# Optimization experiments

Measured on AMD Instinct MI355X. Metric: run time of the kernel, lower is better.

## Reference

```python
import jax, jax.numpy as jnp
import numpy as np

EPS = 1e-5

def _conv3x3(x, w, b):
    # x: [B,C,H,W], w: [O,I,3,3], b: [O]; padding=1 preserves HxW
    y = jax.lax.conv_general_dilated(
        x, w, window_strides=(1, 1), padding=((1, 1), (1, 1)),
        dimension_numbers=('NCHW', 'OIHW', 'NCHW'))
    return y + b[None, :, None, None]

def _instance_norm(x):
    # InstanceNorm2d(affine=False): normalize over spatial dims per (sample, channel)
    mu = jnp.mean(x, axis=(2, 3), keepdims=True)
    var = jnp.var(x, axis=(2, 3), keepdims=True)
    return (x - mu) * jax.lax.rsqrt(var + EPS)

def setup_inputs() -> dict:
    key = jax.random.key(0)
    k1, k2, k3 = jax.random.split(key, 3)
    B, Cin, Cout, H, W = 8, 32, 64, 320, 320
    x = jax.random.normal(k1, (B, Cin, H, W), dtype=jnp.float32)
    w1 = jax.random.normal(k2, (Cout, Cin, 3, 3), dtype=jnp.float32) * (1.0 / np.sqrt(Cin * 9))
    b1 = jnp.zeros((Cout,), dtype=jnp.float32)
    w2 = jax.random.normal(k3, (Cout, Cout, 3, 3), dtype=jnp.float32) * (1.0 / np.sqrt(Cout * 9))
    b2 = jnp.zeros((Cout,), dtype=jnp.float32)
    return {"x": x, "w1": w1, "b1": b1, "w2": w2, "b2": b2}

def reference(x, w1, b1, w2, b2):
    # conv1 -> InstanceNorm -> ReLU -> (Dropout p=0 identity)
    h = jax.nn.relu(_instance_norm(_conv3x3(x, w1, b1)))
    # conv2 -> InstanceNorm -> ReLU -> (Dropout p=0 identity)
    out = jax.nn.relu(_instance_norm(_conv3x3(h, w2, b2)))
    return out
```

## Files before the change

### kernel.cpp

```cpp
#include <hip/hip_runtime.h>

#define HH 320
#define WW 320
#define BB 8
static constexpr float EPS = 1e-5f;

typedef __attribute__((ext_vector_type(8))) short bf16x8;
typedef __attribute__((ext_vector_type(4))) float f32x4;

__device__ inline float bf2f(unsigned short u) {
    union { unsigned int i; float f; } v; v.i = ((unsigned int)u) << 16; return v.f;
}
__device__ inline unsigned short f2bf(float f) {
    union { float f; unsigned int i; } v; v.f = f;
    unsigned int r = v.i + 0x7fffu + ((v.i >> 16) & 1u);
    return (unsigned short)(r >> 16);
}
__device__ inline unsigned int cvtpk(float a, float b) {
    unsigned int r;
    asm volatile("v_cvt_pk_bf16_f32 %0, %1, %2" : "=v"(r) : "v"(a), "v"(b));
    return r;
}
__device__ inline void glds16(const void* g, void* l) {
    __builtin_amdgcn_global_load_lds(
        (const __attribute__((address_space(1))) unsigned int*)g,
        (__attribute__((address_space(3))) unsigned int*)l, 16, 0, 0);
}

__global__ __launch_bounds__(256) void prep_hwc(const float* __restrict__ in,
                                                unsigned short* __restrict__ out)
{
    __shared__ float sT[32][65];
    const int tid = threadIdx.x;
    const int x0  = blockIdx.x * 64;
    const int y   = blockIdx.y;
    const int b   = blockIdx.z;
    for (int e = tid; e < 32 * 64; e += 256) {
        int c = e >> 6, x = e & 63;
        sT[c][x] = in[(((size_t)(b * 32 + c) * HH) + y) * WW + x0 + x];
    }
    __syncthreads();
    for (int e = tid; e < 64 * 32; e += 256) {
        int x = e >> 5, c = e & 31;
        out[((((size_t)b * HH + y) * WW) + x0 + x) * 32 + c] = f2bf(sT[c][x]);
    }
}

__global__ __launch_bounds__(256) void wprep_swz(const float* __restrict__ w1,
                                                 const float* __restrict__ w2,
                                                 unsigned short* __restrict__ wt1,
                                                 unsigned short* __restrict__ wt2)
{
    int i = blockIdx.x * 256 + threadIdx.x;
    if (i < 2304) {
        int s = i & 3, oc = (i >> 2) & 63, kk = i >> 8;
        int icq = s ^ ((oc >> 1) & 3);
        const float* src = w1 + ((size_t)oc * 32 + icq * 8) * 9 + kk;
        unsigned short pk[8];
#pragma unroll
        for (int j = 0; j < 8; ++j) pk[j] = f2bf(src[j * 9]);
        *(bf16x8*)&wt1[(size_t)i * 8] = *(bf16x8*)pk;
    }
    if (i < 4608) {
        int icc = i / 2304, u = i - icc * 2304;
        int s = u & 3, oc = (u >> 2) & 63, kk = u >> 8;
        int icq = s ^ ((oc >> 1) & 3);
        const float* src = w2 + ((size_t)oc * 64 + icc * 32 + icq * 8) * 9 + kk;
        unsigned short pk[8];
#pragma unroll
        for (int j = 0; j < 8; ++j) pk[j] = f2bf(src[j * 9]);
        *(bf16x8*)&wt2[(size_t)i * 8] = *(bf16x8*)pk;
    }
}

__global__ __launch_bounds__(256) void wfold(const unsigned short* __restrict__ wt2,
                                             const float* __restrict__ b2,
                                             const float2* __restrict__ stats1,
                                             unsigned short* __restrict__ wt2b,
                                             float* __restrict__ bias2b)
{
    __shared__ float sMu[64], sR[64];
    __shared__ float sBias[256];
    const int b = blockIdx.x, tid = threadIdx.x;
    if (tid < 64) {
        float2 ms = stats1[b * 64 + tid];
        sMu[tid] = bf2f(f2bf(ms.x));
        sR[tid]  = ms.y;
    }
    __syncthreads();
    const int oc = tid & 63, rep = tid >> 6;
    float bsum = 0.f;
    for (int cs = rep * 2; cs < rep * 2 + 2; ++cs) {
        int icc = cs >> 2, s = cs & 3;
        int icq = s ^ ((oc >> 1) & 3);
        for (int kk = 0; kk < 9; ++kk) {
            size_t u = (size_t)icc * 2304 + kk * 256 + oc * 4 + s;
            bf16x8 v = *(const bf16x8*)&wt2[u * 8];
            unsigned short o8[8];
#pragma unroll
            for (int j = 0; j < 8; ++j) {
                int ic = icc * 32 + icq * 8 + j;
                unsigned short wb = f2bf(bf2f(((unsigned short*)&v)[j]) * sR[ic]);
                o8[j] = wb;
                bsum += bf2f(wb) * sMu[ic];
            }
            *(bf16x8*)&wt2b[((size_t)b * 4608 + u) * 8] = *(bf16x8*)o8;
        }
    }
    sBias[tid] = bsum;
    __syncthreads();
    if (tid < 64) {
        float t = sBias[tid] + sBias[tid + 64] + sBias[tid + 128] + sBias[tid + 192];
        bias2b[b * 64 + tid] = b2[tid] - t;
    }
}

template<int CIN, int NORM>
__global__ __launch_bounds__(256, 3) void conv_mfma(
    const unsigned short* __restrict__ in_hwc,
    const float2* __restrict__ stats_in,
    const unsigned short* __restrict__ wt,
    const float* __restrict__ bias,
    unsigned short* __restrict__ out_hwc,
    float2* __restrict__ partials)
{
    constexpr int ICC = CIN / 32;

    __shared__ __align__(16) char smem[38912];
    unsigned short* sA    = (unsigned short*)smem;
    unsigned short* sW    = (unsigned short*)(smem + 25344);
    float*          sMaxMu= (float*)(smem + 37632);
    unsigned short* sMuBf = (unsigned short*)(smem + 37888);
    float* sRedS  = (float*)smem;
    float* sRedSS = (float*)(smem + 1024);

    const int tid = threadIdx.x;
    const int x0  = blockIdx.x * 64;
    const int y0  = blockIdx.y * 4;
    const int b   = blockIdx.z;
    const int w   = tid >> 6;
    const int l   = tid & 63;
    const int lm  = l & 15;
    const int g   = l >> 4;

    const unsigned short* wtb = NORM ? wt + (size_t)b * 4608 * 8 : wt;
    const float* biasb        = NORM ? bias + b * 64 : bias;

    if (NORM) {
        if (tid < 64) {
            float2 ms = stats_in[b * 64 + tid];
            unsigned short mb = f2bf(ms.x);
            sMuBf[tid]  = mb;
            sMaxMu[tid] = bf2f(mb);
        }
    }

    f32x4 acc[4][4];
#pragma unroll
    for (int fp = 0; fp < 4; ++fp)
#pragma unroll
        for (int fo = 0; fo < 4; ++fo)
            acc[fp][fo] = (f32x4){0.f, 0.f, 0.f, 0.f};

    for (int icc = 0; icc < ICC; ++icc) {
        __syncthreads();

        if (NORM == 0) {
            for (int r = w; r < 6; r += 4) {
                int gy = y0 + r - 1;
                unsigned short* ldsrow = sA + r * 2112;
                if ((unsigned)gy < HH) {
                    const unsigned short* rowbase =
                        in_hwc + ((size_t)(b * HH + gy) * WW) * CIN + icc * 32;
#pragma unroll
                    for (int i = 0; i < 4; ++i) {
                        int u  = 4 + i * 64 + l;
                        int x  = u >> 2;
                        int cs = (u & 3) ^ ((x >> 1) & 3);
                        glds16(rowbase + (size_t)(x0 + x - 1) * CIN + cs * 8,
                               ldsrow + (size_t)(4 + i * 64) * 8);
                    }
                } else {
                    for (int u2 = l; u2 < 264; u2 += 64)
                        *(bf16x8*)(ldsrow + u2 * 8) = (bf16x8){0,0,0,0,0,0,0,0};
                }
            }
            if (tid < 48) {
                int icq = tid & 3, side = (tid >> 2) & 1, r = tid >> 3;
                int xs = side ? 65 : 0;
                int gy = y0 + r - 1, gx = x0 + xs - 1;
                bf16x8 v = (bf16x8){0,0,0,0,0,0,0,0};
                if ((unsigned)gy < HH && (unsigned)gx < WW)
                    v = *(const bf16x8*)&in_hwc[(((size_t)(b * HH + gy) * WW) + gx) * CIN + icc * 32 + icq * 8];
                *(bf16x8*)&sA[(r * 264 + xs * 4 + icq) * 8] = v;
            }
        } else {
#pragma unroll
            for (int k = 0; k < 7; ++k) {
                int e = tid + k * 256;
                if (e < 1584) {
                    int r = e / 264, rem = e - r * 264;
                    int x = rem >> 2, icq = rem & 3;
                    int gy = y0 + r - 1, gx = x0 + x - 1;
                    int c0 = icc * 32 + icq * 8;
                    unsigned int w4[4];
                    if ((unsigned)gy < HH && (unsigned)gx < WW) {
                        bf16x8 v = *(const bf16x8*)&in_hwc[(((size_t)(b * HH + gy) * WW) + gx) * CIN + c0];
#pragma unroll
                        for (int jp = 0; jp < 4; ++jp) {
                            float f0 = fmaxf(bf2f(((unsigned short*)&v)[2 * jp]),     sMaxMu[c0 + 2 * jp]);
                            float f1 = fmaxf(bf2f(((unsigned short*)&v)[2 * jp + 1]), sMaxMu[c0 + 2 * jp + 1]);
                            w4[jp] = cvtpk(f0, f1);
                        }
                    } else {
#pragma unroll
                        for (int jp = 0; jp < 4; ++jp)
                            w4[jp] = (unsigned int)sMuBf[c0 + 2 * jp] |
                                     ((unsigned int)sMuBf[c0 + 2 * jp + 1] << 16);
                    }
                    *(uint4*)&sA[(r * 264 + x * 4 + (icq ^ ((x >> 1) & 3))) * 8] =
                        make_uint4(w4[0], w4[1], w4[2], w4[3]);
                }
            }
        }

#pragma unroll
        for (int kt = 0; kt < 3; ++kt) {
            if (kt > 0) __syncthreads();
            {
                const unsigned short* wsrc = wtb + ((size_t)icc * 2304 + kt * 768) * 8;
#pragma unroll
                for (int k = 0; k < 3; ++k)
                    glds16(wsrc + (size_t)(k * 256 + w * 64 + l) * 8,
                           sW + (size_t)(k * 256 + w * 64) * 8);
            }
            __syncthreads();

            __builtin_amdgcn_s_setprio(1);
#pragma unroll
            for (int kx = 0; kx < 3; ++kx) {
                bf16x8 af[4], bfr[4];
#pragma unroll
                for (int fp = 0; fp < 4; ++fp) {
                    int xl = fp * 16 + lm + kx;
                    int u  = (xl * 4 + g) ^ ((xl >> 1) & 3);
                    af[fp] = *(const bf16x8*)&sA[((w + kt) * 264 + u) * 8];
                }
#pragma unroll
                for (int fo = 0; fo < 4; ++fo) {
                    int ocr = fo * 16 + lm;
                    int p   = (kx * 64 + ocr) * 4 + (g ^ ((ocr >> 1) & 3));
                    bfr[fo] = *(const bf16x8*)&sW[p * 8];
                }
#pragma unroll
                for (int fo = 0; fo < 4; ++fo)
#pragma unroll
                    for (int fp = 0; fp < 4; ++fp)
                        acc[fp][fo] = __builtin_amdgcn_mfma_f32_16x16x32_bf16(
                            bfr[fo], af[fp], acc[fp][fo], 0, 0, 0);
            }
            __builtin_amdgcn_s_setprio(0);
        }
    }

    __syncthreads();

    const int row = y0 + w;
#pragma unroll
    for (int fo = 0; fo < 4; ++fo) {
        float4 b4 = *(const float4*)&biasb[fo * 16 + g * 4];
        float bb[4] = {b4.x, b4.y, b4.z, b4.w};
        float sj[4] = {0,0,0,0}, qj[4] = {0,0,0,0};
#pragma unroll
        for (int fp = 0; fp < 4; ++fp) {
            float v0 = acc[fp][fo][0] + bb[0], v1 = acc[fp][fo][1] + bb[1];
            float v2 = acc[fp][fo][2] + bb[2], v3 = acc[fp][fo][3] + bb[3];
            sj[0] += v0; qj[0] += v0 * v0;  sj[1] += v1; qj[1] += v1 * v1;
            sj[2] += v2; qj[2] += v2 * v2;  sj[3] += v3; qj[3] += v3 * v3;
            uint2 st = make_uint2(cvtpk(v0, v1), cvtpk(v2, v3));
            *(uint2*)&out_hwc[(((size_t)b * HH + row) * WW + x0 + fp * 16 + lm) * 64 + fo * 16 + g * 4] = st;
        }
#pragma unroll
        for (int m = 1; m <= 8; m <<= 1)
#pragma unroll
            for (int j = 0; j < 4; ++j) {
                sj[j] += __shfl_xor(sj[j], m);
                qj[j] += __shfl_xor(qj[j], m);
            }
        if (lm == 0) {
#pragma unroll
            for (int j = 0; j < 4; ++j) {
                sRedS [w * 64 + fo * 16 + g * 4 + j] = sj[j];
                sRedSS[w * 64 + fo * 16 + g * 4 + j] = qj[j];
            }
        }
    }
    __syncthreads();
    if (tid < 64) {
        float S = 0.f, SS = 0.f;
#pragma unroll
        for (int q = 0; q < 4; ++q) { S += sRedS[q * 64 + tid]; SS += sRedSS[q * 64 + tid]; }
        partials[((size_t)b * 400 + blockIdx.y * 5 + blockIdx.x) * 64 + tid] = make_float2(S, SS);
    }
}

__global__ __launch_bounds__(256) void reduce_stats(const float2* __restrict__ partials,
                                                    float2* __restrict__ stats, int count)
{
    const int b  = blockIdx.x;
    const int oc = threadIdx.x & 63;
    const int q  = threadIdx.x >> 6;
    float s = 0.f, ss = 0.f;
    for (int i = q; i < count; i += 4) {
        float2 p = partials[((size_t)b * count + i) * 64 + oc];
        s += p.x; ss += p.y;
    }
    __shared__ float2 red[4][64];
    red[q][oc] = make_float2(s, ss);
    __syncthreads();
    if (threadIdx.x < 64) {
        float S = 0.f, SS = 0.f;
#pragma unroll
        for (int k = 0; k < 4; ++k) { S += red[k][threadIdx.x].x; SS += red[k][threadIdx.x].y; }
        const float n = (float)(HH * WW);
        float mean = S / n;
        float var  = fmaxf(SS / n - mean * mean, 0.f);
        stats[b * 64 + threadIdx.x] = make_float2(mean, rsqrtf(var + EPS));
    }
}

__global__ __launch_bounds__(256) void finalize_t(const unsigned short* __restrict__ h2,
                                                  const float2* __restrict__ stats,
                                                  float* __restrict__ out)
{
    __shared__ float2 sSt[64];
    const int tid = threadIdx.x;
    const int b   = blockIdx.z;
    if (tid < 64) sSt[tid] = stats[b * 64 + tid];
    __syncthreads();
    const int r   = tid >> 6;
    const int px  = tid & 63;
    const int row = blockIdx.y * 4 + r;
    const int x   = blockIdx.x * 64 + px;
    const unsigned short* src = h2 + ((size_t)(b * HH + row) * WW + x) * 64;
    bf16x8 v[8];
#pragma unroll
    for (int cq = 0; cq < 8; ++cq) v[cq] = *(const bf16x8*)(src + cq * 8);
#pragma unroll
    for (int cq = 0; cq < 8; ++cq)
#pragma unroll
        for (int j = 0; j < 8; ++j) {
            int c = cq * 8 + j;
            float2 ms = sSt[c];
            float f = fmaxf((bf2f(((unsigned short*)&v[cq])[j]) - ms.x) * ms.y, 0.f);
            out[((size_t)(b * 64 + c) * HH + row) * WW + x] = f;
        }
}

extern "C" void kernel_launch(void* const* d_in, const int* in_sizes, int n_in,
                              void* d_out, int out_size, void* d_ws, size_t ws_size,
                              hipStream_t stream)
{
    const float* x  = (const float*)d_in[0];
    const float* w1 = (const float*)d_in[1];
    const float* b1 = (const float*)d_in[2];
    const float* w2 = (const float*)d_in[3];
    const float* b2 = (const float*)d_in[4];
    float* out = (float*)d_out;

    char* ws = (char*)d_ws;
    unsigned short* h    = (unsigned short*)ws;
    float2* partials     = (float2*)(ws + 104857600);
    float2* stats1       = (float2*)(ws + 104857600 + 1638400);
    float2* stats2       = (float2*)(ws + 104857600 + 1638400 + 4096);
    unsigned short* reg2 = (unsigned short*)(ws + 104857600 + 1638400 + 8192);
    unsigned short* x_hwc = reg2;
    unsigned short* h2    = reg2;

    char* ob = (char*)d_out + 209715200;
    float*          bias2b = (float*)(ob - 2048);
    unsigned short* wt2b   = (unsigned short*)(ob - 2048 - 589824);
    unsigned short* wt2    = (unsigned short*)(ob - 2048 - 589824 - 73728);
    unsigned short* wt1    = (unsigned short*)(ob - 2048 - 589824 - 73728 - 36864);

    dim3 cgrid(5, 80, BB);

    wprep_swz<<<18, 256, 0, stream>>>(w1, w2, wt1, wt2);
    prep_hwc<<<dim3(5, HH, BB), 256, 0, stream>>>(x, x_hwc);

    conv_mfma<32, 0><<<cgrid, 256, 0, stream>>>(x_hwc, nullptr, wt1, b1, h, partials);
    reduce_stats<<<BB, 256, 0, stream>>>(partials, stats1, 400);
    wfold<<<BB, 256, 0, stream>>>(wt2, b2, stats1, wt2b, bias2b);
    conv_mfma<64, 1><<<cgrid, 256, 0, stream>>>(h, stats1, wt2b, bias2b, h2, partials);
    reduce_stats<<<BB, 256, 0, stream>>>(partials, stats2, 400);
    finalize_t<<<dim3(5, 80, BB), 256, 0, stream>>>(h2, stats2, out);
}
```

Before: 365.5 us.

## Double-buffer conv input and weight slabs and process four row tiles per block

The conv kernel now loops over four 4-row tiles per block (grid y shrinks from 80 to 20) and double-buffers both the activation tile and the weight slab in LDS. The next slab and the next input group are prefetched while MFMAs run on the current one, and for the normalized conv the global loads are held in registers and written to LDS after compute. Per-block statistics are accumulated across tiles, so the partials count drops to 100 per sample. The aim is to hide global load latency and cut the number of barriers per MFMA. The cost is higher LDS use, a lower occupancy hint (2 blocks instead of 3) and fewer blocks in the grid.

```diff
diff --git a/kernel.cpp b/kernel.cpp
--- a/kernel.cpp
+++ b/kernel.cpp
@@ -116,7 +116,7 @@
 }
 
 template<int CIN, int NORM>
-__global__ __launch_bounds__(256, 3) void conv_mfma(
+__global__ __launch_bounds__(256, 2) void conv_mfma(
     const unsigned short* __restrict__ in_hwc,
     const float2* __restrict__ stats_in,
     const unsigned short* __restrict__ wt,
@@ -125,18 +125,19 @@
     float2* __restrict__ partials)
 {
     constexpr int ICC = CIN / 32;
-
-    __shared__ __align__(16) char smem[38912];
-    unsigned short* sA    = (unsigned short*)smem;
-    unsigned short* sW    = (unsigned short*)(smem + 25344);
-    float*          sMaxMu= (float*)(smem + 37632);
-    unsigned short* sMuBf = (unsigned short*)(smem + 37888);
-    float* sRedS  = (float*)smem;
-    float* sRedSS = (float*)(smem + 1024);
+    constexpr int NG  = 4 * ICC;
+    constexpr int NS  = NG * 3;
+
+    __shared__ __align__(16) unsigned short sA[2][6 * 264 * 8];
+    __shared__ __align__(16) unsigned short sWb[2][768 * 8];
+    __shared__ float sRedS[256];
+    __shared__ float sRedSS[256];
+    __shared__ float sMaxMu[64];
+    __shared__ unsigned short sMuBf[64];
 
     const int tid = threadIdx.x;
     const int x0  = blockIdx.x * 64;
-    const int y0  = blockIdx.y * 4;
+    const int yb  = blockIdx.y * 16;
     const int b   = blockIdx.z;
     const int w   = tid >> 6;
     const int l   = tid & 63;
@@ -153,7 +154,101 @@
             sMuBf[tid]  = mb;
             sMaxMu[tid] = bf2f(mb);
         }
-    }
+        __syncthreads();
+    }
+
+    auto stage_slab = [&](int s2, int buf) {
+        int kt2  = s2 % 3;
+        int icc2 = (s2 / 3) % ICC;
+        const unsigned short* wsrc = wtb + ((size_t)icc2 * 2304 + kt2 * 768) * 8;
+        unsigned short* dst = &sWb[buf][0];
+#pragma unroll
+        for (int k = 0; k < 3; ++k)
+            glds16(wsrc + (size_t)(k * 256 + w * 64 + l) * 8,
+                   dst + (size_t)(k * 256 + w * 64) * 8);
+    };
+
+    auto issueA_glds = [&](int gi2) {
+        int t2 = gi2 / ICC, icc2 = gi2 % ICC;
+        int y02 = yb + t2 * 4;
+        unsigned short* buf = &sA[gi2 & 1][0];
+        for (int r = w; r < 6; r += 4) {
+            int gy = y02 + r - 1;
+            unsigned short* ldsrow = buf + r * 2112;
+            if ((unsigned)gy < HH) {
+                const unsigned short* rowbase =
+                    in_hwc + ((size_t)(b * HH + gy) * WW) * CIN + icc2 * 32;
+#pragma unroll
+                for (int i = 0; i < 4; ++i) {
+                    int u  = 4 + i * 64 + l;
+                    int x  = u >> 2;
+                    int cs = (u & 3) ^ ((x >> 1) & 3);
+                    glds16(rowbase + (size_t)(x0 + x - 1) * CIN + cs * 8,
+                           ldsrow + (size_t)(4 + i * 64) * 8);
+                }
+            } else {
+                for (int u2 = l; u2 < 264; u2 += 64)
+                    *(bf16x8*)(ldsrow + u2 * 8) = (bf16x8){0,0,0,0,0,0,0,0};
+            }
+        }
+        if (tid < 48) {
+            int icq = tid & 3, side = (tid >> 2) & 1, r = tid >> 3;
+            int xs = side ? 65 : 0;
+            int gy = y02 + r - 1, gx = x0 + xs - 1;
+            bf16x8 v = (bf16x8){0,0,0,0,0,0,0,0};
+            if ((unsigned)gy < HH && (unsigned)gx < WW)
+                v = *(const bf16x8*)&in_hwc[(((size_t)(b * HH + gy) * WW) + gx) * CIN + icc2 * 32 + icq * 8];
+            *(bf16x8*)&buf[(r * 264 + xs * 4 + icq) * 8] = v;
+        }
+    };
+
+    bf16x8 ld[7];
+    auto issueA_reg = [&](int gi2) {
+        int t2 = gi2 / ICC, icc2 = gi2 % ICC;
+        int y02 = yb + t2 * 4;
+#pragma unroll
+        for (int k = 0; k < 7; ++k) {
+            int e = tid + k * 256;
+            if (e < 1584) {
+                int r = e / 264, rem = e - r * 264;
+                int x = rem >> 2, icq = rem & 3;
+                int gy = y02 + r - 1, gx = x0 + x - 1;
+                if ((unsigned)gy < HH && (unsigned)gx < WW)
+                    ld[k] = *(const bf16x8*)&in_hwc[(((size_t)(b * HH + gy) * WW) + gx) * CIN + icc2 * 32 + icq * 8];
+            }
+        }
+    };
+    auto writeA_reg = [&](int gi2) {
+        int t2 = gi2 / ICC, icc2 = gi2 % ICC;
+        int y02 = yb + t2 * 4;
+        unsigned short* buf = &sA[gi2 & 1][0];
+#pragma unroll
+        for (int k = 0; k < 7; ++k) {
+            int e = tid + k * 256;
+            if (e < 1584) {
+                int r = e / 264, rem = e - r * 264;
+                int x = rem >> 2, icq = rem & 3;
+                int gy = y02 + r - 1, gx = x0 + x - 1;
+                int c0 = icc2 * 32 + icq * 8;
+                unsigned int w4[4];
+                if ((unsigned)gy < HH && (unsigned)gx < WW) {
+#pragma unroll
+                    for (int jp = 0; jp < 4; ++jp) {
+                        float f0 = fmaxf(bf2f(((unsigned short*)&ld[k])[2 * jp]),     sMaxMu[c0 + 2 * jp]);
+                        float f1 = fmaxf(bf2f(((unsigned short*)&ld[k])[2 * jp + 1]), sMaxMu[c0 + 2 * jp + 1]);
+                        w4[jp] = cvtpk(f0, f1);
+                    }
+                } else {
+#pragma unroll
+                    for (int jp = 0; jp < 4; ++jp)
+                        w4[jp] = (unsigned int)sMuBf[c0 + 2 * jp] |
+                                 ((unsigned int)sMuBf[c0 + 2 * jp + 1] << 16);
+                }
+                *(uint4*)&buf[(r * 264 + x * 4 + (icq ^ ((x >> 1) & 3))) * 8] =
+                    make_uint4(w4[0], w4[1], w4[2], w4[3]);
+            }
+        }
+    };
 
     f32x4 acc[4][4];
 #pragma unroll
@@ -162,80 +257,38 @@
         for (int fo = 0; fo < 4; ++fo)
             acc[fp][fo] = (f32x4){0.f, 0.f, 0.f, 0.f};
 
-    for (int icc = 0; icc < ICC; ++icc) {
-        __syncthreads();
-
-        if (NORM == 0) {
-            for (int r = w; r < 6; r += 4) {
-                int gy = y0 + r - 1;
-                unsigned short* ldsrow = sA + r * 2112;
-                if ((unsigned)gy < HH) {
-                    const unsigned short* rowbase =
-                        in_hwc + ((size_t)(b * HH + gy) * WW) * CIN + icc * 32;
-#pragma unroll
-                    for (int i = 0; i < 4; ++i) {
-                        int u  = 4 + i * 64 + l;
-                        int x  = u >> 2;
-                        int cs = (u & 3) ^ ((x >> 1) & 3);
-                        glds16(rowbase + (size_t)(x0 + x - 1) * CIN + cs * 8,
-                               ldsrow + (size_t)(4 + i * 64) * 8);
-                    }
-                } else {
-                    for (int u2 = l; u2 < 264; u2 += 64)
-                        *(bf16x8*)(ldsrow + u2 * 8) = (bf16x8){0,0,0,0,0,0,0,0};
-                }
-            }
-            if (tid < 48) {
-                int icq = tid & 3, side = (tid >> 2) & 1, r = tid >> 3;
-                int xs = side ? 65 : 0;
-                int gy = y0 + r - 1, gx = x0 + xs - 1;
-                bf16x8 v = (bf16x8){0,0,0,0,0,0,0,0};
-                if ((unsigned)gy < HH && (unsigned)gx < WW)
-                    v = *(const bf16x8*)&in_hwc[(((size_t)(b * HH + gy) * WW) + gx) * CIN + icc * 32 + icq * 8];
-                *(bf16x8*)&sA[(r * 264 + xs * 4 + icq) * 8] = v;
-            }
-        } else {
-#pragma unroll
-            for (int k = 0; k < 7; ++k) {
-                int e = tid + k * 256;
-                if (e < 1584) {
-                    int r = e / 264, rem = e - r * 264;
-                    int x = rem >> 2, icq = rem & 3;
-                    int gy = y0 + r - 1, gx = x0 + x - 1;
-                    int c0 = icc * 32 + icq * 8;
-                    unsigned int w4[4];
-                    if ((unsigned)gy < HH && (unsigned)gx < WW) {
-                        bf16x8 v = *(const bf16x8*)&in_hwc[(((size_t)(b * HH + gy) * WW) + gx) * CIN + c0];
-#pragma unroll
-                        for (int jp = 0; jp < 4; ++jp) {
-                            float f0 = fmaxf(bf2f(((unsigned short*)&v)[2 * jp]),     sMaxMu[c0 + 2 * jp]);
-                            float f1 = fmaxf(bf2f(((unsigned short*)&v)[2 * jp + 1]), sMaxMu[c0 + 2 * jp + 1]);
-                            w4[jp] = cvtpk(f0, f1);
-                        }
-                    } else {
-#pragma unroll
-                        for (int jp = 0; jp < 4; ++jp)
-                            w4[jp] = (unsigned int)sMuBf[c0 + 2 * jp] |
-                                     ((unsigned int)sMuBf[c0 + 2 * jp + 1] << 16);
-                    }
-                    *(uint4*)&sA[(r * 264 + x * 4 + (icq ^ ((x >> 1) & 3))) * 8] =
-                        make_uint4(w4[0], w4[1], w4[2], w4[3]);
-                }
-            }
-        }
-
-#pragma unroll
-        for (int kt = 0; kt < 3; ++kt) {
-            if (kt > 0) __syncthreads();
-            {
-                const unsigned short* wsrc = wtb + ((size_t)icc * 2304 + kt * 768) * 8;
-#pragma unroll
-                for (int k = 0; k < 3; ++k)
-                    glds16(wsrc + (size_t)(k * 256 + w * 64 + l) * 8,
-                           sW + (size_t)(k * 256 + w * 64) * 8);
-            }
-            __syncthreads();
-
+    float bb[4][4];
+#pragma unroll
+    for (int fo = 0; fo < 4; ++fo) {
+        float4 b4 = *(const float4*)&biasb[fo * 16 + g * 4];
+        bb[fo][0] = b4.x; bb[fo][1] = b4.y; bb[fo][2] = b4.z; bb[fo][3] = b4.w;
+    }
+    float sjA[4][4] = {}, qjA[4][4] = {};
+
+    stage_slab(0, 0);
+    if (NORM == 0) {
+        issueA_glds(0);
+    } else {
+        issueA_reg(0);
+        writeA_reg(0);
+    }
+    __syncthreads();
+
+    for (int s = 0; s < NS; ++s) {
+        const int kt = s % 3;
+        const int gi = s / 3;
+        const int icc = gi % ICC;
+        const int t  = gi / ICC;
+
+        if (s + 1 < NS) stage_slab(s + 1, (s + 1) & 1);
+        if (kt == 0 && gi + 1 < NG) {
+            if (NORM == 0) issueA_glds(gi + 1);
+            else           issueA_reg(gi + 1);
+        }
+
+        {
+            const unsigned short* bufA = &sA[gi & 1][0];
+            const unsigned short* bufW = &sWb[s & 1][0];
             __builtin_amdgcn_s_setprio(1);
 #pragma unroll
             for (int kx = 0; kx < 3; ++kx) {
@@ -244,13 +297,13 @@
                 for (int fp = 0; fp < 4; ++fp) {
                     int xl = fp * 16 + lm + kx;
                     int u  = (xl * 4 + g) ^ ((xl >> 1) & 3);
-                    af[fp] = *(const bf16x8*)&sA[((w + kt) * 264 + u) * 8];
+                    af[fp] = *(const bf16x8*)(bufA + ((w + kt) * 264 + u) * 8);
                 }
 #pragma unroll
                 for (int fo = 0; fo < 4; ++fo) {
                     int ocr = fo * 16 + lm;
                     int p   = (kx * 64 + ocr) * 4 + (g ^ ((ocr >> 1) & 3));
-                    bfr[fo] = *(const bf16x8*)&sW[p * 8];
+                    bfr[fo] = *(const bf16x8*)(bufW + p * 8);
                 }
 #pragma unroll
                 for (int fo = 0; fo < 4; ++fo)
@@ -261,37 +314,45 @@
             }
             __builtin_amdgcn_s_setprio(0);
         }
-    }
-
-    __syncthreads();
-
-    const int row = y0 + w;
+
+        if (kt == 2 && icc == ICC - 1) {
+            const int row = yb + 4 * t + w;
+#pragma unroll
+            for (int fo = 0; fo < 4; ++fo) {
+#pragma unroll
+                for (int fp = 0; fp < 4; ++fp) {
+                    float v0 = acc[fp][fo][0] + bb[fo][0], v1 = acc[fp][fo][1] + bb[fo][1];
+                    float v2 = acc[fp][fo][2] + bb[fo][2], v3 = acc[fp][fo][3] + bb[fo][3];
+                    sjA[fo][0] += v0; qjA[fo][0] += v0 * v0;
+                    sjA[fo][1] += v1; qjA[fo][1] += v1 * v1;
+                    sjA[fo][2] += v2; qjA[fo][2] += v2 * v2;
+                    sjA[fo][3] += v3; qjA[fo][3] += v3 * v3;
+                    uint2 st = make_uint2(cvtpk(v0, v1), cvtpk(v2, v3));
+                    *(uint2*)&out_hwc[(((size_t)b * HH + row) * WW + x0 + fp * 16 + lm) * 64 + fo * 16 + g * 4] = st;
+                    acc[fp][fo] = (f32x4){0.f, 0.f, 0.f, 0.f};
+                }
+            }
+        }
+
+        if (NORM == 1 && kt == 2 && gi + 1 < NG) writeA_reg(gi + 1);
+
+        __syncthreads();
+    }
+
 #pragma unroll
     for (int fo = 0; fo < 4; ++fo) {
-        float4 b4 = *(const float4*)&biasb[fo * 16 + g * 4];
-        float bb[4] = {b4.x, b4.y, b4.z, b4.w};
-        float sj[4] = {0,0,0,0}, qj[4] = {0,0,0,0};
-#pragma unroll
-        for (int fp = 0; fp < 4; ++fp) {
-            float v0 = acc[fp][fo][0] + bb[0], v1 = acc[fp][fo][1] + bb[1];
-            float v2 = acc[fp][fo][2] + bb[2], v3 = acc[fp][fo][3] + bb[3];
-            sj[0] += v0; qj[0] += v0 * v0;  sj[1] += v1; qj[1] += v1 * v1;
-            sj[2] += v2; qj[2] += v2 * v2;  sj[3] += v3; qj[3] += v3 * v3;
-            uint2 st = make_uint2(cvtpk(v0, v1), cvtpk(v2, v3));
-            *(uint2*)&out_hwc[(((size_t)b * HH + row) * WW + x0 + fp * 16 + lm) * 64 + fo * 16 + g * 4] = st;
-        }
 #pragma unroll
         for (int m = 1; m <= 8; m <<= 1)
 #pragma unroll
             for (int j = 0; j < 4; ++j) {
-                sj[j] += __shfl_xor(sj[j], m);
-                qj[j] += __shfl_xor(qj[j], m);
+                sjA[fo][j] += __shfl_xor(sjA[fo][j], m);
+                qjA[fo][j] += __shfl_xor(qjA[fo][j], m);
             }
         if (lm == 0) {
 #pragma unroll
             for (int j = 0; j < 4; ++j) {
-                sRedS [w * 64 + fo * 16 + g * 4 + j] = sj[j];
-                sRedSS[w * 64 + fo * 16 + g * 4 + j] = qj[j];
+                sRedS [w * 64 + fo * 16 + g * 4 + j] = sjA[fo][j];
+                sRedSS[w * 64 + fo * 16 + g * 4 + j] = qjA[fo][j];
             }
         }
     }
@@ -300,7 +361,7 @@
         float S = 0.f, SS = 0.f;
 #pragma unroll
         for (int q = 0; q < 4; ++q) { S += sRedS[q * 64 + tid]; SS += sRedSS[q * 64 + tid]; }
-        partials[((size_t)b * 400 + blockIdx.y * 5 + blockIdx.x) * 64 + tid] = make_float2(S, SS);
+        partials[((size_t)b * 100 + blockIdx.y * 5 + blockIdx.x) * 64 + tid] = make_float2(S, SS);
     }
 }
 
@@ -383,15 +444,15 @@
     unsigned short* wt2    = (unsigned short*)(ob - 2048 - 589824 - 73728);
     unsigned short* wt1    = (unsigned short*)(ob - 2048 - 589824 - 73728 - 36864);
 
-    dim3 cgrid(5, 80, BB);
+    dim3 cgrid(5, 20, BB);
 
     wprep_swz<<<18, 256, 0, stream>>>(w1, w2, wt1, wt2);
     prep_hwc<<<dim3(5, HH, BB), 256, 0, stream>>>(x, x_hwc);
 
     conv_mfma<32, 0><<<cgrid, 256, 0, stream>>>(x_hwc, nullptr, wt1, b1, h, partials);
-    reduce_stats<<<BB, 256, 0, stream>>>(partials, stats1, 400);
+    reduce_stats<<<BB, 256, 0, stream>>>(partials, stats1, 100);
     wfold<<<BB, 256, 0, stream>>>(wt2, b2, stats1, wt2b, bias2b);
     conv_mfma<64, 1><<<cgrid, 256, 0, stream>>>(h, stats1, wt2b, bias2b, h2, partials);
-    reduce_stats<<<BB, 256, 0, stream>>>(partials, stats2, 400);
+    reduce_stats<<<BB, 256, 0, stream>>>(partials, stats2, 100);
     finalize_t<<<dim3(5, 80, BB), 256, 0, stream>>>(h2, stats2, out);
 }
```

Result: faster. 323.2 us, median of 2 (-11.6%).

## Double-buffer conv1 over 16-row supertiles and fuse stats reduction into weight fold

Applied to the files above, without the earlier changes.

Conv1 now runs as a persistent-style block covering 16 output rows (four 4-row groups). Its input tiles and weight slabs are double-buffered in LDS so the loads for the next step overlap the MFMA work of the current one, and per-block stats partials drop from 400 to 100 per sample. The separate reduce_stats launch for conv1 is merged into the weight-fold kernel, which saves one launch. The cost is that conv1 grid parallelism falls to 800 blocks with higher LDS use (2 waves per SIMD occupancy bound), which may leave CUs underfilled.

```diff
diff --git a/kernel.cpp b/kernel.cpp
--- a/kernel.cpp
+++ b/kernel.cpp
@@ -73,28 +73,46 @@
     }
 }
 
-__global__ __launch_bounds__(256) void wfold(const unsigned short* __restrict__ wt2,
-                                             const float* __restrict__ b2,
-                                             const float2* __restrict__ stats1,
-                                             unsigned short* __restrict__ wt2b,
-                                             float* __restrict__ bias2b)
-{
+__global__ __launch_bounds__(256) void fold_stats(const float2* __restrict__ partials,
+                                                  const float* __restrict__ b2,
+                                                  const unsigned short* __restrict__ wt2,
+                                                  float2* __restrict__ stats1,
+                                                  unsigned short* __restrict__ wt2b,
+                                                  float* __restrict__ bias2b)
+{
+    __shared__ float2 red[4][64];
     __shared__ float sMu[64], sR[64];
     __shared__ float sBias[256];
     const int b = blockIdx.x, tid = threadIdx.x;
+    const int oc = tid & 63, q = tid >> 6;
+
+    float s = 0.f, ss = 0.f;
+    for (int i = q; i < 100; i += 4) {
+        float2 p = partials[((size_t)b * 100 + i) * 64 + oc];
+        s += p.x; ss += p.y;
+    }
+    red[q][oc] = make_float2(s, ss);
+    __syncthreads();
     if (tid < 64) {
-        float2 ms = stats1[b * 64 + tid];
-        sMu[tid] = bf2f(f2bf(ms.x));
-        sR[tid]  = ms.y;
-    }
-    __syncthreads();
-    const int oc = tid & 63, rep = tid >> 6;
+        float S = 0.f, SS = 0.f;
+#pragma unroll
+        for (int k = 0; k < 4; ++k) { S += red[k][tid].x; SS += red[k][tid].y; }
+        const float n = (float)(HH * WW);
+        float mean = S / n;
+        float var  = fmaxf(SS / n - mean * mean, 0.f);
+        float rstd = rsqrtf(var + EPS);
+        stats1[b * 64 + tid] = make_float2(mean, rstd);
+        sMu[tid] = bf2f(f2bf(mean));
+        sR[tid]  = rstd;
+    }
+    __syncthreads();
+
     float bsum = 0.f;
-    for (int cs = rep * 2; cs < rep * 2 + 2; ++cs) {
-        int icc = cs >> 2, s = cs & 3;
-        int icq = s ^ ((oc >> 1) & 3);
+    for (int cs = q * 2; cs < q * 2 + 2; ++cs) {
+        int icc = cs >> 2, sdx = cs & 3;
+        int icq = sdx ^ ((oc >> 1) & 3);
         for (int kk = 0; kk < 9; ++kk) {
-            size_t u = (size_t)icc * 2304 + kk * 256 + oc * 4 + s;
+            size_t u = (size_t)icc * 2304 + kk * 256 + oc * 4 + sdx;
             bf16x8 v = *(const bf16x8*)&wt2[u * 8];
             unsigned short o8[8];
 #pragma unroll
@@ -115,8 +133,176 @@
     }
 }
 
-template<int CIN, int NORM>
-__global__ __launch_bounds__(256, 3) void conv_mfma(
+__global__ __launch_bounds__(256, 2) void conv1_super(
+    const unsigned short* __restrict__ in_hwc,
+    const unsigned short* __restrict__ wt,
+    const float* __restrict__ bias,
+    unsigned short* __restrict__ out_hwc,
+    float2* __restrict__ partials)
+{
+    constexpr int NG = 4;
+    constexpr int NS = 12;
+
+    __shared__ __align__(16) unsigned short sA[2][6 * 264 * 8];
+    __shared__ __align__(16) unsigned short sWb[2][768 * 8];
+    __shared__ float sRedS[256];
+    __shared__ float sRedSS[256];
+
+    const int tid = threadIdx.x;
+    const int x0  = blockIdx.x * 64;
+    const int yb  = blockIdx.y * 16;
+    const int b   = blockIdx.z;
+    const int w   = tid >> 6;
+    const int l   = tid & 63;
+    const int lm  = l & 15;
+    const int g   = l >> 4;
+
+    auto stage_slab = [&](int s2, int buf) {
+        int kt2 = s2 % 3;
+        const unsigned short* wsrc = wt + (size_t)(kt2 * 768) * 8;
+        unsigned short* dst = &sWb[buf][0];
+#pragma unroll
+        for (int k = 0; k < 3; ++k)
+            glds16(wsrc + (size_t)(k * 256 + w * 64 + l) * 8,
+                   dst + (size_t)(k * 256 + w * 64) * 8);
+    };
+
+    auto issueA_glds = [&](int gi2) {
+        int y02 = yb + gi2 * 4;
+        unsigned short* buf = &sA[gi2 & 1][0];
+        for (int r = w; r < 6; r += 4) {
+            int gy = y02 + r - 1;
+            unsigned short* ldsrow = buf + r * 2112;
+            if ((unsigned)gy < HH) {
+                const unsigned short* rowbase =
+                    in_hwc + ((size_t)(b * HH + gy) * WW) * 32;
+#pragma unroll
+                for (int i = 0; i < 4; ++i) {
+                    int u  = 4 + i * 64 + l;
+                    int x  = u >> 2;
+                    int cs = (u & 3) ^ ((x >> 1) & 3);
+                    glds16(rowbase + (size_t)(x0 + x - 1) * 32 + cs * 8,
+                           ldsrow + (size_t)(4 + i * 64) * 8);
+                }
+            } else {
+                for (int u2 = l; u2 < 264; u2 += 64)
+                    *(bf16x8*)(ldsrow + u2 * 8) = (bf16x8){0,0,0,0,0,0,0,0};
+            }
+        }
+        if (tid < 48) {
+            int icq = tid & 3, side = (tid >> 2) & 1, r = tid >> 3;
+            int xs = side ? 65 : 0;
+            int gy = y02 + r - 1, gx = x0 + xs - 1;
+            bf16x8 v = (bf16x8){0,0,0,0,0,0,0,0};
+            if ((unsigned)gy < HH && (unsigned)gx < WW)
+                v = *(const bf16x8*)&in_hwc[(((size_t)(b * HH + gy) * WW) + gx) * 32 + icq * 8];
+            *(bf16x8*)&buf[(r * 264 + xs * 4 + icq) * 8] = v;
+        }
+    };
+
+    f32x4 acc[4][4];
+#pragma unroll
+    for (int fp = 0; fp < 4; ++fp)
+#pragma unroll
+        for (int fo = 0; fo < 4; ++fo)
+            acc[fp][fo] = (f32x4){0.f, 0.f, 0.f, 0.f};
+
+    float bb[4][4];
+#pragma unroll
+    for (int fo = 0; fo < 4; ++fo) {
+        float4 b4 = *(const float4*)&bias[fo * 16 + g * 4];
+        bb[fo][0] = b4.x; bb[fo][1] = b4.y; bb[fo][2] = b4.z; bb[fo][3] = b4.w;
+    }
+    float sjA[4][4] = {}, qjA[4][4] = {};
+
+    stage_slab(0, 0);
+    issueA_glds(0);
+    __syncthreads();
+
+    for (int s = 0; s < NS; ++s) {
+        const int kt = s % 3;
+        const int gi = s / 3;
+
+        if (s + 1 < NS) stage_slab(s + 1, (s + 1) & 1);
+        if (kt == 0 && gi + 1 < NG) issueA_glds(gi + 1);
+
+        {
+            const unsigned short* bufA = &sA[gi & 1][0];
+            const unsigned short* bufW = &sWb[s & 1][0];
+            __builtin_amdgcn_s_setprio(1);
+#pragma unroll
+            for (int kx = 0; kx < 3; ++kx) {
+                bf16x8 af[4], bfr[4];
+#pragma unroll
+                for (int fp = 0; fp < 4; ++fp) {
+                    int xl = fp * 16 + lm + kx;
+                    int u  = (xl * 4 + g) ^ ((xl >> 1) & 3);
+                    af[fp] = *(const bf16x8*)(bufA + ((w + kt) * 264 + u) * 8);
+                }
+#pragma unroll
+                for (int fo = 0; fo < 4; ++fo) {
+                    int ocr = fo * 16 + lm;
+                    int p   = (kx * 64 + ocr) * 4 + (g ^ ((ocr >> 1) & 3));
+                    bfr[fo] = *(const bf16x8*)(bufW + p * 8);
+                }
+#pragma unroll
+                for (int fo = 0; fo < 4; ++fo)
+#pragma unroll
+                    for (int fp = 0; fp < 4; ++fp)
+                        acc[fp][fo] = __builtin_amdgcn_mfma_f32_16x16x32_bf16(
+                            bfr[fo], af[fp], acc[fp][fo], 0, 0, 0);
+            }
+            __builtin_amdgcn_s_setprio(0);
+        }
+
+        if (kt == 2) {
+            const int row = yb + 4 * gi + w;
+#pragma unroll
+            for (int fo = 0; fo < 4; ++fo) {
+#pragma unroll
+                for (int fp = 0; fp < 4; ++fp) {
+                    float v0 = acc[fp][fo][0] + bb[fo][0], v1 = acc[fp][fo][1] + bb[fo][1];
+                    float v2 = acc[fp][fo][2] + bb[fo][2], v3 = acc[fp][fo][3] + bb[fo][3];
+                    sjA[fo][0] += v0; qjA[fo][0] += v0 * v0;
+                    sjA[fo][1] += v1; qjA[fo][1] += v1 * v1;
+                    sjA[fo][2] += v2; qjA[fo][2] += v2 * v2;
+                    sjA[fo][3] += v3; qjA[fo][3] += v3 * v3;
+                    uint2 st = make_uint2(cvtpk(v0, v1), cvtpk(v2, v3));
+                    *(uint2*)&out_hwc[(((size_t)b * HH + row) * WW + x0 + fp * 16 + lm) * 64 + fo * 16 + g * 4] = st;
+                    acc[fp][fo] = (f32x4){0.f, 0.f, 0.f, 0.f};
+                }
+            }
+        }
+        __syncthreads();
+    }
+
+#pragma unroll
+    for (int fo = 0; fo < 4; ++fo) {
+#pragma unroll
+        for (int m = 1; m <= 8; m <<= 1)
+#pragma unroll
+            for (int j = 0; j < 4; ++j) {
+                sjA[fo][j] += __shfl_xor(sjA[fo][j], m);
+                qjA[fo][j] += __shfl_xor(qjA[fo][j], m);
+            }
+        if (lm == 0) {
+#pragma unroll
+            for (int j = 0; j < 4; ++j) {
+                sRedS [w * 64 + fo * 16 + g * 4 + j] = sjA[fo][j];
+                sRedSS[w * 64 + fo * 16 + g * 4 + j] = qjA[fo][j];
+            }
+        }
+    }
+    __syncthreads();
+    if (tid < 64) {
+        float S = 0.f, SS = 0.f;
+#pragma unroll
+        for (int q = 0; q < 4; ++q) { S += sRedS[q * 64 + tid]; SS += sRedSS[q * 64 + tid]; }
+        partials[((size_t)b * 100 + blockIdx.y * 5 + blockIdx.x) * 64 + tid] = make_float2(S, SS);
+    }
+}
+
+__global__ __launch_bounds__(256, 3) void conv2_tile(
     const unsigned short* __restrict__ in_hwc,
     const float2* __restrict__ stats_in,
     const unsigned short* __restrict__ wt,
@@ -124,8 +310,6 @@
     unsigned short* __restrict__ out_hwc,
     float2* __restrict__ partials)
 {
-    constexpr int ICC = CIN / 32;
-
     __shared__ __align__(16) char smem[38912];
     unsigned short* sA    = (unsigned short*)smem;
     unsigned short* sW    = (unsigned short*)(smem + 25344);
@@ -143,16 +327,14 @@
     const int lm  = l & 15;
     const int g   = l >> 4;
 
-    const unsigned short* wtb = NORM ? wt + (size_t)b * 4608 * 8 : wt;
-    const float* biasb        = NORM ? bias + b * 64 : bias;
-
-    if (NORM) {
-        if (tid < 64) {
-            float2 ms = stats_in[b * 64 + tid];
-            unsigned short mb = f2bf(ms.x);
-            sMuBf[tid]  = mb;
-            sMaxMu[tid] = bf2f(mb);
-        }
+    const unsigned short* wtb = wt + (size_t)b * 4608 * 8;
+    const float* biasb        = bias + b * 64;
+
+    if (tid < 64) {
+        float2 ms = stats_in[b * 64 + tid];
+        unsigned short mb = f2bf(ms.x);
+        sMuBf[tid]  = mb;
+        sMaxMu[tid] = bf2f(mb);
     }
 
     f32x4 acc[4][4];
@@ -162,65 +344,34 @@
         for (int fo = 0; fo < 4; ++fo)
             acc[fp][fo] = (f32x4){0.f, 0.f, 0.f, 0.f};
 
-    for (int icc = 0; icc < ICC; ++icc) {
+    for (int icc = 0; icc < 2; ++icc) {
         __syncthreads();
 
-        if (NORM == 0) {
-            for (int r = w; r < 6; r += 4) {
-                int gy = y0 + r - 1;
-                unsigned short* ldsrow = sA + r * 2112;
-                if ((unsigned)gy < HH) {
-                    const unsigned short* rowbase =
-                        in_hwc + ((size_t)(b * HH + gy) * WW) * CIN + icc * 32;
-#pragma unroll
-                    for (int i = 0; i < 4; ++i) {
-                        int u  = 4 + i * 64 + l;
-                        int x  = u >> 2;
-                        int cs = (u & 3) ^ ((x >> 1) & 3);
-                        glds16(rowbase + (size_t)(x0 + x - 1) * CIN + cs * 8,
-                               ldsrow + (size_t)(4 + i * 64) * 8);
+#pragma unroll
+        for (int k = 0; k < 7; ++k) {
+            int e = tid + k * 256;
+            if (e < 1584) {
+                int r = e / 264, rem = e - r * 264;
+                int x = rem >> 2, icq = rem & 3;
+                int gy = y0 + r - 1, gx = x0 + x - 1;
+                int c0 = icc * 32 + icq * 8;
+                unsigned int w4[4];
+                if ((unsigned)gy < HH && (unsigned)gx < WW) {
+                    bf16x8 v = *(const bf16x8*)&in_hwc[(((size_t)(b * HH + gy) * WW) + gx) * 64 + c0];
+#pragma unroll
+                    for (int jp = 0; jp < 4; ++jp) {
+                        float f0 = fmaxf(bf2f(((unsigned short*)&v)[2 * jp]),     sMaxMu[c0 + 2 * jp]);
+                        float f1 = fmaxf(bf2f(((unsigned short*)&v)[2 * jp + 1]), sMaxMu[c0 + 2 * jp + 1]);
+                        w4[jp] = cvtpk(f0, f1);
                     }
                 } else {
-                    for (int u2 = l; u2 < 264; u2 += 64)
-                        *(bf16x8*)(ldsrow + u2 * 8) = (bf16x8){0,0,0,0,0,0,0,0};
-                }
-            }
-            if (tid < 48) {
-                int icq = tid & 3, side = (tid >> 2) & 1, r = tid >> 3;
-                int xs = side ? 65 : 0;
-                int gy = y0 + r - 1, gx = x0 + xs - 1;
-                bf16x8 v = (bf16x8){0,0,0,0,0,0,0,0};
-                if ((unsigned)gy < HH && (unsigned)gx < WW)
-                    v = *(const bf16x8*)&in_hwc[(((size_t)(b * HH + gy) * WW) + gx) * CIN + icc * 32 + icq * 8];
-                *(bf16x8*)&sA[(r * 264 + xs * 4 + icq) * 8] = v;
-            }
-        } else {
-#pragma unroll
-            for (int k = 0; k < 7; ++k) {
-                int e = tid + k * 256;
-                if (e < 1584) {
-                    int r = e / 264, rem = e - r * 264;
-                    int x = rem >> 2, icq = rem & 3;
-                    int gy = y0 + r - 1, gx = x0 + x - 1;
-                    int c0 = icc * 32 + icq * 8;
-                    unsigned int w4[4];
-                    if ((unsigned)gy < HH && (unsigned)gx < WW) {
-                        bf16x8 v = *(const bf16x8*)&in_hwc[(((size_t)(b * HH + gy) * WW) + gx) * CIN + c0];
-#pragma unroll
-                        for (int jp = 0; jp < 4; ++jp) {
-                            float f0 = fmaxf(bf2f(((unsigned short*)&v)[2 * jp]),     sMaxMu[c0 + 2 * jp]);
-                            float f1 = fmaxf(bf2f(((unsigned short*)&v)[2 * jp + 1]), sMaxMu[c0 + 2 * jp + 1]);
-                            w4[jp] = cvtpk(f0, f1);
-                        }
-                    } else {
-#pragma unroll
-                        for (int jp = 0; jp < 4; ++jp)
-                            w4[jp] = (unsigned int)sMuBf[c0 + 2 * jp] |
-                                     ((unsigned int)sMuBf[c0 + 2 * jp + 1] << 16);
-                    }
-                    *(uint4*)&sA[(r * 264 + x * 4 + (icq ^ ((x >> 1) & 3))) * 8] =
-                        make_uint4(w4[0], w4[1], w4[2], w4[3]);
-                }
+#pragma unroll
+                    for (int jp = 0; jp < 4; ++jp)
+                        w4[jp] = (unsigned int)sMuBf[c0 + 2 * jp] |
+                                 ((unsigned int)sMuBf[c0 + 2 * jp + 1] << 16);
+                }
+                *(uint4*)&sA[(r * 264 + x * 4 + (icq ^ ((x >> 1) & 3))) * 8] =
+                    make_uint4(w4[0], w4[1], w4[2], w4[3]);
             }
         }
 
@@ -249,7 +400,7 @@
 #pragma unroll
                 for (int fo = 0; fo < 4; ++fo) {
                     int ocr = fo * 16 + lm;
-                    int p   = (kx * 64 + ocr) * 4 + (g ^ ((ocr >> 1) & 3));
+                    int p   = (kx * 256 + ocr * 4 + (g ^ ((ocr >> 1) & 3)));
                     bfr[fo] = *(const bf16x8*)&sW[p * 8];
                 }
 #pragma unroll
@@ -383,15 +534,12 @@
     unsigned short* wt2    = (unsigned short*)(ob - 2048 - 589824 - 73728);
     unsigned short* wt1    = (unsigned short*)(ob - 2048 - 589824 - 73728 - 36864);
 
-    dim3 cgrid(5, 80, BB);
-
     wprep_swz<<<18, 256, 0, stream>>>(w1, w2, wt1, wt2);
     prep_hwc<<<dim3(5, HH, BB), 256, 0, stream>>>(x, x_hwc);
 
-    conv_mfma<32, 0><<<cgrid, 256, 0, stream>>>(x_hwc, nullptr, wt1, b1, h, partials);
-    reduce_stats<<<BB, 256, 0, stream>>>(partials, stats1, 400);
-    wfold<<<BB, 256, 0, stream>>>(wt2, b2, stats1, wt2b, bias2b);
-    conv_mfma<64, 1><<<cgrid, 256, 0, stream>>>(h, stats1, wt2b, bias2b, h2, partials);
+    conv1_super<<<dim3(5, 20, BB), 256, 0, stream>>>(x_hwc, wt1, b1, h, partials);
+    fold_stats<<<BB, 256, 0, stream>>>(partials, b2, wt2, stats1, wt2b, bias2b);
+    conv2_tile<<<dim3(5, 80, BB), 256, 0, stream>>>(h, stats1, wt2b, bias2b, h2, partials);
     reduce_stats<<<BB, 256, 0, stream>>>(partials, stats2, 400);
     finalize_t<<<dim3(5, 80, BB), 256, 0, stream>>>(h2, stats2, out);
 }
```

New measurement: 334.4 us. 1.09x faster.
